# Kernel optimization log

Hardware: AMD Instinct MI355X
Metric: run time of the kernel (lower is better)

Reference implementation:

```python
import jax, jax.numpy as jnp
import numpy as np

B, T, V, E, H, D = 2048, 50, 65, 100, 20, 5  # batch, block, vocab, n_embd, heads, head_size


def setup_inputs() -> dict:
    key = jax.random.key(0)
    ks = jax.random.split(key, 12)
    idx = jax.random.randint(ks[0], (B, T), 0, V)
    targets = jax.random.randint(ks[1], (B, T), 0, V)
    tok_emb = jax.random.normal(ks[2], (V, E), dtype=jnp.float32) * 0.02
    pos_emb = jax.random.normal(ks[3], (T, E), dtype=jnp.float32) * 0.02
    # per-head Linear(N_EMBD, head_size, bias=False) weights, stacked over heads: [H, D, E]
    Wk = jax.random.normal(ks[4], (H, D, E), dtype=jnp.float32) * 0.1
    Wq = jax.random.normal(ks[5], (H, D, E), dtype=jnp.float32) * 0.1
    Wv = jax.random.normal(ks[6], (H, D, E), dtype=jnp.float32) * 0.1
    W_ff = jax.random.normal(ks[7], (E, E), dtype=jnp.float32) * 0.1
    b_ff = jnp.zeros((E,), dtype=jnp.float32)
    W_lm = jax.random.normal(ks[8], (V, E), dtype=jnp.float32) * 0.1
    b_lm = jnp.zeros((V,), dtype=jnp.float32)
    return {"idx": idx, "targets": targets, "tok_emb": tok_emb, "pos_emb": pos_emb,
            "Wk": Wk, "Wq": Wq, "Wv": Wv, "W_ff": W_ff, "b_ff": b_ff,
            "W_lm": W_lm, "b_lm": b_lm}


def reference(idx, targets, tok_emb, pos_emb, Wk, Wq, Wv, W_ff, b_ff, W_lm, b_lm):
    Bs, Ts = idx.shape
    x = tok_emb[idx] + pos_emb[:Ts]  # [B, T, E]
    # batched over all heads (equivalent to the per-head Python loop + concat)
    k = jnp.einsum('bte,hde->bhtd', x, Wk)
    q = jnp.einsum('bte,hde->bhtd', x, Wq)
    v = jnp.einsum('bte,hde->bhtd', x, Wv)
    # NOTE: faithful to original: k @ q^T, scaled by C**0.5 (multiply, C = N_EMBD)
    scale = jnp.asarray(E, x.dtype) ** 0.5
    w = jnp.einsum('bhtd,bhsd->bhts', k, q) * scale  # [B, H, T, S]
    tril = jnp.tril(jnp.ones((Ts, Ts), dtype=bool))
    w = jnp.where(tril, w, -jnp.inf)
    # original: torch.softmax(weights, dim=1) on [B, T, S] -> axis 't' here (axis=2)
    w = jax.nn.softmax(w, axis=2)
    attn = jnp.einsum('bhts,bhsd->bhtd', w, v)
    attn = attn.transpose(0, 2, 1, 3).reshape(Bs, Ts, H * D)  # concat heads -> [B, T, E]
    h = jax.nn.relu(attn @ W_ff.T + b_ff)  # FeedForward applied AFTER attention
    logits = h @ W_lm.T + b_lm  # [B, T, V]
    logits2d = logits.reshape(Bs * Ts, V)
    tflat = targets.reshape(Bs * Ts)
    logp = jax.nn.log_softmax(logits2d, axis=-1)
    loss = -jnp.take_along_axis(logp, tflat[:, None], axis=-1).mean()
    return (logits2d, loss)
```

## Files before the change

kernel.cpp:

```cpp
#include <hip/hip_runtime.h>
#include <hip/hip_bf16.h>

#define Bb 2048
#define Tt 50
#define Vv 65
#define Ee 100
#define Hh 20
#define Dd 5

typedef __bf16 v8bf __attribute__((ext_vector_type(8)));
typedef short v8s __attribute__((ext_vector_type(8)));
typedef short v4s __attribute__((ext_vector_type(4)));
typedef float f32x4 __attribute__((ext_vector_type(4)));

__device__ __forceinline__ v8bf bzero8() {
    v8s z = {0, 0, 0, 0, 0, 0, 0, 0};
    union { v8s s; v8bf b; } u; u.s = z; return u.b;
}
__device__ __forceinline__ unsigned short bfbits(float f) {
    union { __hip_bfloat16 h; unsigned short s; } c;
    c.h = __float2bfloat16(f);
    return c.s;
}
__device__ __forceinline__ float bf2f(short s) {
    union { unsigned i; float f; } c; c.i = ((unsigned)(unsigned short)s) << 16; return c.f;
}
__device__ __forceinline__ unsigned pack2(float a, float b) {
    return (unsigned)bfbits(a) | ((unsigned)bfbits(b) << 16);
}

__device__ __forceinline__ f32x4 mfma_16x16x16_bf16(v4s a, v4s b, f32x4 c) {
#if __has_builtin(__builtin_amdgcn_mfma_f32_16x16x16bf16_1k)
    return __builtin_amdgcn_mfma_f32_16x16x16bf16_1k(a, b, c, 0, 0, 0);
#else
    f32x4 d;
    asm volatile("v_mfma_f32_16x16x16_bf16 %0, %1, %2, %3\n\ts_nop 7\n\ts_nop 4"
                 : "=v"(d) : "v"(a), "v"(b), "v"(c));
    return d;
#endif
}

#define WS_WKQV 1024
#define WS_WFF  (1024 + 81920)
#define WS_WLM  (1024 + 81920 + 32768)
#define WS_LPART (1024 + 81920 + 32768 + 20480)

#define XSTR 136
#define R2 8000
#define R3 16000

__global__ __launch_bounds__(256) void prep_kernel(
    const float* __restrict__ Wk, const float* __restrict__ Wq,
    const float* __restrict__ Wv, const float* __restrict__ Wff,
    const float* __restrict__ Wlm, char* __restrict__ ws)
{
    int g = blockIdx.x * 256 + threadIdx.x;
    __hip_bfloat16* wkqv = (__hip_bfloat16*)(ws + WS_WKQV);
    __hip_bfloat16* wff  = (__hip_bfloat16*)(ws + WS_WFF);
    __hip_bfloat16* wlm  = (__hip_bfloat16*)(ws + WS_WLM);
    if (g < 40960) {
        int n = g >> 7, e = g & 127;
        float v = 0.f;
        if (e < Ee) {
            if (n < 100)      v = Wk[n * Ee + e] * 14.4269504089f;
            else if (n < 200) v = Wq[(n - 100) * Ee + e];
            else if (n < 300) v = Wv[(n - 200) * Ee + e];
        }
        wkqv[g] = __float2bfloat16(v);
    } else if (g < 57344) {
        int gg = g - 40960; int n = gg >> 7, e = gg & 127;
        float v = (e < Ee && n < Ee) ? Wff[n * Ee + e] : 0.f;
        wff[gg] = __float2bfloat16(v);
    } else {
        int gg = g - 57344; int n = gg >> 7, e = gg & 127;
        float v = (e < Ee && n < Vv) ? Wlm[n * Ee + e] : 0.f;
        wlm[gg] = __float2bfloat16(v);
    }
}

__global__ __launch_bounds__(256, 3) void gpt_main(
    const int* __restrict__ idx, const int* __restrict__ targets,
    const float* __restrict__ tok_emb, const float* __restrict__ pos_emb,
    const float* __restrict__ b_ff, const float* __restrict__ b_lm,
    const char* __restrict__ ws, float* __restrict__ out,
    float* __restrict__ loss_part)
{
    __shared__ __attribute__((aligned(16))) __hip_bfloat16 sh[22400];
    __shared__ int tok_s[Tt];
    __shared__ float bsum;

    const int b    = blockIdx.x;
    const int tid  = threadIdx.x;
    const int wave = tid >> 6;
    const int ln   = tid & 15;
    const int quad = (tid >> 4) & 3;

    if (tid < Tt) tok_s[tid] = idx[b * Tt + tid];
    if (tid == 0) bsum = 0.f;
    {
        const uint4 z4 = make_uint4(0u, 0u, 0u, 0u);
        for (int i = tid; i < 2800; i += 256) ((uint4*)sh)[i] = z4;
    }
    __syncthreads();
    for (int i = tid; i < Tt * 25; i += 256) {
        int r = i / 25, c4 = (i - r * 25) * 4;
        const float4 te = *(const float4*)&tok_emb[tok_s[r] * Ee + c4];
        const float4 pe = *(const float4*)&pos_emb[r * Ee + c4];
        ushort4 o;
        o.x = bfbits(te.x + pe.x); o.y = bfbits(te.y + pe.y);
        o.z = bfbits(te.z + pe.z); o.w = bfbits(te.w + pe.w);
        *(ushort4*)&sh[r * XSTR + c4] = o;
    }
    __syncthreads();

    {
        const __hip_bfloat16* wkqv = (const __hip_bfloat16*)(ws + WS_WKQV);
        f32x4 acc[5][4];
#pragma unroll
        for (int j = 0; j < 5; ++j)
#pragma unroll
            for (int mt = 0; mt < 4; ++mt) {
                f32x4 z = {0.f, 0.f, 0.f, 0.f};
                acc[j][mt] = z;
            }
#pragma unroll
        for (int kt = 0; kt < 4; ++kt) {
            v8bf a[4];
#pragma unroll
            for (int mt = 0; mt < 4; ++mt)
                a[mt] = (mt < 3 || ln < 2)
                      ? *(const v8bf*)&sh[(mt * 16 + ln) * XSTR + kt * 32 + quad * 8]
                      : bzero8();
#pragma unroll
            for (int j = 0; j < 5; ++j) {
                int nt = wave * 5 + j;
                v8bf bfr = *(const v8bf*)&wkqv[(nt * 16 + ln) * 128 + kt * 32 + quad * 8];
#pragma unroll
                for (int mt = 0; mt < 4; ++mt)
                    acc[j][mt] = __builtin_amdgcn_mfma_f32_16x16x32_bf16(a[mt], bfr, acc[j][mt], 0, 0, 0);
            }
        }
        __syncthreads();
        for (int i = tid; i < 1000; i += 256) {
            *(unsigned short*)&sh[i * 8 + 5] = 0;
            *(unsigned*)&sh[i * 8 + 6] = 0;
        }
#pragma unroll
        for (int j = 0; j < 5; ++j) {
            int n = (wave * 5 + j) * 16 + ln;
            if (n < 300) {
                int mat = n / 100;
                int jj  = n - mat * 100;
                int h   = jj / 5, d = jj - (jj / 5) * 5;
#pragma unroll
                for (int mt = 0; mt < 4; ++mt)
#pragma unroll
                    for (int r = 0; r < 4; ++r) {
                        int m = mt * 16 + quad * 4 + r;
                        if (m < Tt) {
                            __hip_bfloat16 val = __float2bfloat16(acc[j][mt][r]);
                            if (mat == 0)      sh[R2 + (h * 50 + m) * 8 + d] = val;
                            else if (mat == 1) sh[(h * 50 + m) * 8 + d] = val;
                            else               sh[R3 + (h * 5 + d) * 64 + m] = val;
                        }
                    }
            }
        }
    }
    __syncthreads();

    unsigned attp[5][8];
    {
        v4s ones4; ones4[0] = ones4[1] = ones4[2] = ones4[3] = (short)0x3F80;
#pragma unroll
        for (int hj = 0; hj < 5; ++hj) {
            const int h = wave * 5 + hj;
            v8bf qf[4], kf[4];
#pragma unroll
            for (int i = 0; i < 4; ++i) {
                int row = i * 16 + ln;
                qf[i] = (quad == 0) ? *(const v8bf*)&sh[(h * 50 + row) * 8] : bzero8();
                kf[i] = (quad == 0) ? *(const v8bf*)&sh[R2 + (h * 50 + row) * 8] : bzero8();
            }
            float rdv[4][4];
#pragma unroll
            for (int ns = 0; ns < 4; ++ns) {
                float esum[4] = {0.f, 0.f, 0.f, 0.f};
#pragma unroll
                for (int mt = ns; mt < 4; ++mt) {
                    f32x4 z = {0.f, 0.f, 0.f, 0.f};
                    f32x4 t2 = __builtin_amdgcn_mfma_f32_16x16x32_bf16(kf[mt], qf[ns], z, 0, 0, 0);
                    int s = ns * 16 + ln;
#pragma unroll
                    for (int r = 0; r < 4; ++r) {
                        int t = mt * 16 + quad * 4 + r;
                        float x = __builtin_amdgcn_exp2f(t2[r]);
                        esum[r] += (t >= s && t < Tt && s < Tt) ? x : 0.f;
                    }
                }
                v4s af;
                af[0] = (short)bfbits(esum[0]); af[1] = (short)bfbits(esum[1]);
                af[2] = (short)bfbits(esum[2]); af[3] = (short)bfbits(esum[3]);
                f32x4 z = {0.f, 0.f, 0.f, 0.f};
                f32x4 dres = mfma_16x16x16_bf16(af, ones4, z);
#pragma unroll
                for (int r = 0; r < 4; ++r) {
                    int s = ns * 16 + quad * 4 + r;
                    rdv[ns][r] = (s < Tt) ? __builtin_amdgcn_rcpf(dres[r]) : 0.f;
                }
            }
            f32x4 pac[4];
#pragma unroll
            for (int mt = 0; mt < 4; ++mt) { f32x4 z = {0.f, 0.f, 0.f, 0.f}; pac[mt] = z; }
#pragma unroll
            for (int ms = 0; ms < 4; ++ms) {
                v4s braw;
                if (ln < Dd) braw = *(const v4s*)&sh[R3 + (h * 5 + ln) * 64 + ms * 16 + quad * 4];
                else { v4s z = {0, 0, 0, 0}; braw = z; }
                v4s bvt;
#pragma unroll
                for (int j = 0; j < 4; ++j)
                    bvt[j] = (short)bfbits(bf2f(braw[j]) * rdv[ms][j]);
#pragma unroll
                for (int u = 0; u < 4 - ms; ++u) {
                    f32x4 z = {0.f, 0.f, 0.f, 0.f};
                    f32x4 t1 = __builtin_amdgcn_mfma_f32_16x16x32_bf16(qf[ms], kf[ms + u], z, 0, 0, 0);
                    int t = (ms + u) * 16 + ln;
                    v4s af;
#pragma unroll
                    for (int r = 0; r < 4; ++r) {
                        int s = ms * 16 + quad * 4 + r;
                        float x = __builtin_amdgcn_exp2f(t1[r]);
                        x = (t >= s && t < Tt && s < Tt) ? x : 0.f;
                        af[r] = (short)bfbits(x);
                    }
                    pac[ms + u] = mfma_16x16x16_bf16(af, bvt, pac[ms + u]);
                }
            }
#pragma unroll
            for (int mt = 0; mt < 4; ++mt) {
                attp[hj][mt * 2]     = pack2(pac[mt][0], pac[mt][1]);
                attp[hj][mt * 2 + 1] = pack2(pac[mt][2], pac[mt][3]);
            }
        }
    }
    __syncthreads();

#pragma unroll
    for (int hj = 0; hj < 5; ++hj) {
        int col = (wave * 5 + hj) * 5 + ln;
#pragma unroll
        for (int mt = 0; mt < 4; ++mt)
#pragma unroll
            for (int r = 0; r < 4; ++r) {
                int t = mt * 16 + quad * 4 + r;
                if (ln < Dd && t < Tt) {
                    unsigned w = attp[hj][mt * 2 + (r >> 1)];
                    unsigned short v = (unsigned short)((r & 1) ? (w >> 16) : (w & 0xffff));
                    *(unsigned short*)&sh[t * XSTR + col] = v;
                }
            }
    }
    __syncthreads();

    {
        const __hip_bfloat16* wff = (const __hip_bfloat16*)(ws + WS_WFF);
        f32x4 fac[2][4];
#pragma unroll
        for (int u = 0; u < 2; ++u)
#pragma unroll
            for (int mt = 0; mt < 4; ++mt) {
                f32x4 z = {0.f, 0.f, 0.f, 0.f};
                fac[u][mt] = z;
            }
        const int nn = (wave < 3) ? 2 : 1;
#pragma unroll
        for (int kt = 0; kt < 4; ++kt) {
            v8bf a[4];
#pragma unroll
            for (int mt = 0; mt < 4; ++mt)
                a[mt] = (mt < 3 || ln < 2)
                      ? *(const v8bf*)&sh[(mt * 16 + ln) * XSTR + kt * 32 + quad * 8]
                      : bzero8();
#pragma unroll
            for (int u = 0; u < 2; ++u) {
                if (u < nn) {
                    int nt = wave + u * 4;
                    v8bf bfr = *(const v8bf*)&wff[(nt * 16 + ln) * 128 + kt * 32 + quad * 8];
#pragma unroll
                    for (int mt = 0; mt < 4; ++mt)
                        fac[u][mt] = __builtin_amdgcn_mfma_f32_16x16x32_bf16(a[mt], bfr, fac[u][mt], 0, 0, 0);
                }
            }
        }
#pragma unroll
        for (int u = 0; u < 2; ++u) {
            if (u < nn) {
                int n = (wave + u * 4) * 16 + ln;
                if (n < Ee) {
                    float bias = b_ff[n];
#pragma unroll
                    for (int mt = 0; mt < 4; ++mt)
#pragma unroll
                        for (int r = 0; r < 4; ++r) {
                            int m = mt * 16 + quad * 4 + r;
                            if (m < Tt) {
                                float v = fac[u][mt][r] + bias;
                                sh[R2 + m * XSTR + n] = __float2bfloat16(v > 0.f ? v : 0.f);
                            }
                        }
                }
            }
        }
    }
    __syncthreads();

    {
        const __hip_bfloat16* wlm = (const __hip_bfloat16*)(ws + WS_WLM);
        float* lgl = (float*)sh;
#pragma unroll
        for (int i = 0; i < 5; ++i) {
            int job = wave + i * 4;
            int mt = job / 5, nt = job - (job / 5) * 5;
            f32x4 acc = {0.f, 0.f, 0.f, 0.f};
#pragma unroll
            for (int kt = 0; kt < 4; ++kt) {
                v8bf a = (mt < 3 || ln < 2)
                       ? *(const v8bf*)&sh[R2 + (mt * 16 + ln) * XSTR + kt * 32 + quad * 8]
                       : bzero8();
                v8bf bf = *(const v8bf*)&wlm[(nt * 16 + ln) * 128 + kt * 32 + quad * 8];
                acc = __builtin_amdgcn_mfma_f32_16x16x32_bf16(a, bf, acc, 0, 0, 0);
            }
            int n = nt * 16 + ln;
            if (n < Vv) {
                float bias = b_lm[n];
#pragma unroll
                for (int r = 0; r < 4; ++r) {
                    int m = mt * 16 + quad * 4 + r;
                    if (m < Tt) {
                        float v = acc[r] + bias;
                        out[(b * Tt + m) * Vv + n] = v;
                        lgl[m * 68 + n] = v;
                    }
                }
            }
        }
    }
    __syncthreads();

    if (tid < 200) {
        int r = tid >> 2, lv = tid & 3;
        const float* row = (const float*)sh + r * 68;
        float mx = -3.0e38f;
        for (int v = lv; v < Vv; v += 4) mx = fmaxf(mx, row[v]);
        mx = fmaxf(mx, __shfl_xor(mx, 1));
        mx = fmaxf(mx, __shfl_xor(mx, 2));
        float sum = 0.f;
        for (int v = lv; v < Vv; v += 4)
            sum += __builtin_amdgcn_exp2f((row[v] - mx) * 1.4426950408889634f);
        sum += __shfl_xor(sum, 1);
        sum += __shfl_xor(sum, 2);
        if (lv == 0) {
            float lse = mx + 0.69314718055994531f * log2f(sum);
            int tgt = targets[b * Tt + r];
            atomicAdd(&bsum, lse - row[tgt]);
        }
    }
    __syncthreads();
    if (tid == 0) loss_part[b] = bsum;
}

__global__ __launch_bounds__(256) void loss_reduce(const float* __restrict__ lp,
                                                   float* __restrict__ out)
{
    __shared__ float wsum[4];
    int tid = threadIdx.x;
    float s = 0.f;
    for (int i = tid; i < Bb; i += 256) s += lp[i];
    s += __shfl_xor(s, 1);  s += __shfl_xor(s, 2);  s += __shfl_xor(s, 4);
    s += __shfl_xor(s, 8);  s += __shfl_xor(s, 16); s += __shfl_xor(s, 32);
    if ((tid & 63) == 0) wsum[tid >> 6] = s;
    __syncthreads();
    if (tid == 0)
        out[Bb * Tt * Vv] = (wsum[0] + wsum[1] + wsum[2] + wsum[3]) * (1.0f / (float)(Bb * Tt));
}

extern "C" void kernel_launch(void* const* d_in, const int* in_sizes, int n_in,
                              void* d_out, int out_size, void* d_ws, size_t ws_size,
                              hipStream_t stream)
{
    const int* idx     = (const int*)d_in[0];
    const int* targets = (const int*)d_in[1];
    const float* tok_emb = (const float*)d_in[2];
    const float* pos_emb = (const float*)d_in[3];
    const float* Wk  = (const float*)d_in[4];
    const float* Wq  = (const float*)d_in[5];
    const float* Wv  = (const float*)d_in[6];
    const float* Wff = (const float*)d_in[7];
    const float* bff = (const float*)d_in[8];
    const float* Wlm = (const float*)d_in[9];
    const float* blm = (const float*)d_in[10];
    float* out = (float*)d_out;
    char* ws = (char*)d_ws;
    float* loss_part = (float*)(ws + WS_LPART);

    hipLaunchKernelGGL(prep_kernel, dim3(264), dim3(256), 0, stream, Wk, Wq, Wv, Wff, Wlm, ws);
    hipLaunchKernelGGL(gpt_main, dim3(Bb), dim3(256), 0, stream,
                       idx, targets, tok_emb, pos_emb, bff, blm, (const char*)ws, out, loss_part);
    hipLaunchKernelGGL(loss_reduce, dim3(1), dim3(256), 0, stream, loss_part, out);
}
```

Measured before the change: 188.1 us.

## Store Q/K in fp8 and shrink shared memory to fit more blocks per CU

Q and K projections are now stored in LDS as fp8 e4m3 and the attention score MFMAs use the fp8 variant. The log2e·sqrt(E) scaling is split evenly across Wk and Wq so both sit in a reasonable fp8 range. The LDS buffer is re-laid out as bytes and shrunk from about 44.8KB to 28.8KB, and launch bounds rise from 3 to 5 blocks per CU to improve occupancy. This risks precision loss in the attention scores, since fp8 has a 3-bit mantissa and the scores are scaled by about 14.4 before exp2.

```diff
diff --git a/kernel.cpp b/kernel.cpp
--- a/kernel.cpp
+++ b/kernel.cpp
@@ -1,5 +1,6 @@
 #include <hip/hip_runtime.h>
 #include <hip/hip_bf16.h>
+#include <hip/hip_fp8.h>
 
 #define Bb 2048
 #define Tt 50
@@ -27,6 +28,15 @@
 }
 __device__ __forceinline__ unsigned pack2(float a, float b) {
     return (unsigned)bfbits(a) | ((unsigned)bfbits(b) << 16);
+}
+__device__ __forceinline__ unsigned char f32_to_fp8(float v) {
+#if __has_builtin(__builtin_amdgcn_cvt_pk_fp8_f32)
+    return (unsigned char)(__builtin_amdgcn_cvt_pk_fp8_f32(v, 0.f, 0, false) & 0xff);
+#else
+    union { __hip_fp8_e4m3 t; unsigned char c; } u;
+    u.t = __hip_fp8_e4m3(v);
+    return u.c;
+#endif
 }
 
 __device__ __forceinline__ f32x4 mfma_16x16x16_bf16(v4s a, v4s b, f32x4 c) {
@@ -45,9 +55,10 @@
 #define WS_WLM  (1024 + 81920 + 32768)
 #define WS_LPART (1024 + 81920 + 32768 + 20480)
 
-#define XSTR 136
-#define R2 8000
-#define R3 16000
+#define KB8 8000
+#define VTB 16000
+#define HB  13600
+#define XROW 272
 
 __global__ __launch_bounds__(256) void prep_kernel(
     const float* __restrict__ Wk, const float* __restrict__ Wq,
@@ -62,8 +73,8 @@
         int n = g >> 7, e = g & 127;
         float v = 0.f;
         if (e < Ee) {
-            if (n < 100)      v = Wk[n * Ee + e] * 14.4269504089f;
-            else if (n < 200) v = Wq[(n - 100) * Ee + e];
+            if (n < 100)      v = Wk[n * Ee + e] * 3.7982825f;
+            else if (n < 200) v = Wq[(n - 100) * Ee + e] * 3.7982825f;
             else if (n < 300) v = Wv[(n - 200) * Ee + e];
         }
         wkqv[g] = __float2bfloat16(v);
@@ -78,14 +89,14 @@
     }
 }
 
-__global__ __launch_bounds__(256, 3) void gpt_main(
+__global__ __launch_bounds__(256, 5) void gpt_main(
     const int* __restrict__ idx, const int* __restrict__ targets,
     const float* __restrict__ tok_emb, const float* __restrict__ pos_emb,
     const float* __restrict__ b_ff, const float* __restrict__ b_lm,
     const char* __restrict__ ws, float* __restrict__ out,
     float* __restrict__ loss_part)
 {
-    __shared__ __attribute__((aligned(16))) __hip_bfloat16 sh[22400];
+    __shared__ __attribute__((aligned(16))) unsigned char shB[28800];
     __shared__ int tok_s[Tt];
     __shared__ float bsum;
 
@@ -99,7 +110,7 @@
     if (tid == 0) bsum = 0.f;
     {
         const uint4 z4 = make_uint4(0u, 0u, 0u, 0u);
-        for (int i = tid; i < 2800; i += 256) ((uint4*)sh)[i] = z4;
+        for (int i = tid; i < 1800; i += 256) ((uint4*)shB)[i] = z4;
     }
     __syncthreads();
     for (int i = tid; i < Tt * 25; i += 256) {
@@ -109,7 +120,7 @@
         ushort4 o;
         o.x = bfbits(te.x + pe.x); o.y = bfbits(te.y + pe.y);
         o.z = bfbits(te.z + pe.z); o.w = bfbits(te.w + pe.w);
-        *(ushort4*)&sh[r * XSTR + c4] = o;
+        *(ushort4*)&shB[r * XROW + c4 * 2] = o;
     }
     __syncthreads();
 
@@ -129,7 +140,7 @@
 #pragma unroll
             for (int mt = 0; mt < 4; ++mt)
                 a[mt] = (mt < 3 || ln < 2)
-                      ? *(const v8bf*)&sh[(mt * 16 + ln) * XSTR + kt * 32 + quad * 8]
+                      ? *(const v8bf*)&shB[(mt * 16 + ln) * XROW + (kt * 32 + quad * 8) * 2]
                       : bzero8();
 #pragma unroll
             for (int j = 0; j < 5; ++j) {
@@ -142,8 +153,8 @@
         }
         __syncthreads();
         for (int i = tid; i < 1000; i += 256) {
-            *(unsigned short*)&sh[i * 8 + 5] = 0;
-            *(unsigned*)&sh[i * 8 + 6] = 0;
+            shB[i * 8 + 5] = 0; *(unsigned short*)&shB[i * 8 + 6] = 0;
+            shB[KB8 + i * 8 + 5] = 0; *(unsigned short*)&shB[KB8 + i * 8 + 6] = 0;
         }
 #pragma unroll
         for (int j = 0; j < 5; ++j) {
@@ -158,10 +169,10 @@
                     for (int r = 0; r < 4; ++r) {
                         int m = mt * 16 + quad * 4 + r;
                         if (m < Tt) {
-                            __hip_bfloat16 val = __float2bfloat16(acc[j][mt][r]);
-                            if (mat == 0)      sh[R2 + (h * 50 + m) * 8 + d] = val;
-                            else if (mat == 1) sh[(h * 50 + m) * 8 + d] = val;
-                            else               sh[R3 + (h * 5 + d) * 64 + m] = val;
+                            float v = acc[j][mt][r];
+                            if (mat == 0)      shB[KB8 + (h * 50 + m) * 8 + d] = f32_to_fp8(v);
+                            else if (mat == 1) shB[(h * 50 + m) * 8 + d] = f32_to_fp8(v);
+                            else *(unsigned short*)&shB[VTB + ((h * 5 + d) * 64 + m) * 2] = bfbits(v);
                         }
                     }
             }
@@ -175,12 +186,12 @@
 #pragma unroll
         for (int hj = 0; hj < 5; ++hj) {
             const int h = wave * 5 + hj;
-            v8bf qf[4], kf[4];
+            long qf[4], kf[4];
 #pragma unroll
             for (int i = 0; i < 4; ++i) {
                 int row = i * 16 + ln;
-                qf[i] = (quad == 0) ? *(const v8bf*)&sh[(h * 50 + row) * 8] : bzero8();
-                kf[i] = (quad == 0) ? *(const v8bf*)&sh[R2 + (h * 50 + row) * 8] : bzero8();
+                qf[i] = (quad == 0) ? *(const long*)&shB[(h * 50 + row) * 8] : 0L;
+                kf[i] = (quad == 0) ? *(const long*)&shB[KB8 + (h * 50 + row) * 8] : 0L;
             }
             float rdv[4][4];
 #pragma unroll
@@ -189,7 +200,7 @@
 #pragma unroll
                 for (int mt = ns; mt < 4; ++mt) {
                     f32x4 z = {0.f, 0.f, 0.f, 0.f};
-                    f32x4 t2 = __builtin_amdgcn_mfma_f32_16x16x32_bf16(kf[mt], qf[ns], z, 0, 0, 0);
+                    f32x4 t2 = __builtin_amdgcn_mfma_f32_16x16x32_fp8_fp8(kf[mt], qf[ns], z, 0, 0, 0);
                     int s = ns * 16 + ln;
 #pragma unroll
                     for (int r = 0; r < 4; ++r) {
@@ -215,7 +226,7 @@
 #pragma unroll
             for (int ms = 0; ms < 4; ++ms) {
                 v4s braw;
-                if (ln < Dd) braw = *(const v4s*)&sh[R3 + (h * 5 + ln) * 64 + ms * 16 + quad * 4];
+                if (ln < Dd) braw = *(const v4s*)&shB[VTB + ((h * 5 + ln) * 64 + ms * 16 + quad * 4) * 2];
                 else { v4s z = {0, 0, 0, 0}; braw = z; }
                 v4s bvt;
 #pragma unroll
@@ -224,7 +235,7 @@
 #pragma unroll
                 for (int u = 0; u < 4 - ms; ++u) {
                     f32x4 z = {0.f, 0.f, 0.f, 0.f};
-                    f32x4 t1 = __builtin_amdgcn_mfma_f32_16x16x32_bf16(qf[ms], kf[ms + u], z, 0, 0, 0);
+                    f32x4 t1 = __builtin_amdgcn_mfma_f32_16x16x32_fp8_fp8(qf[ms], kf[ms + u], z, 0, 0, 0);
                     int t = (ms + u) * 16 + ln;
                     v4s af;
 #pragma unroll
@@ -257,7 +268,7 @@
                 if (ln < Dd && t < Tt) {
                     unsigned w = attp[hj][mt * 2 + (r >> 1)];
                     unsigned short v = (unsigned short)((r & 1) ? (w >> 16) : (w & 0xffff));
-                    *(unsigned short*)&sh[t * XSTR + col] = v;
+                    *(unsigned short*)&shB[t * XROW + col * 2] = v;
                 }
             }
     }
@@ -280,7 +291,7 @@
 #pragma unroll
             for (int mt = 0; mt < 4; ++mt)
                 a[mt] = (mt < 3 || ln < 2)
-                      ? *(const v8bf*)&sh[(mt * 16 + ln) * XSTR + kt * 32 + quad * 8]
+                      ? *(const v8bf*)&shB[(mt * 16 + ln) * XROW + (kt * 32 + quad * 8) * 2]
                       : bzero8();
 #pragma unroll
             for (int u = 0; u < 2; ++u) {
@@ -306,7 +317,8 @@
                             int m = mt * 16 + quad * 4 + r;
                             if (m < Tt) {
                                 float v = fac[u][mt][r] + bias;
-                                sh[R2 + m * XSTR + n] = __float2bfloat16(v > 0.f ? v : 0.f);
+                                *(unsigned short*)&shB[HB + m * XROW + n * 2] =
+                                    bfbits(v > 0.f ? v : 0.f);
                             }
                         }
                 }
@@ -317,7 +329,7 @@
 
     {
         const __hip_bfloat16* wlm = (const __hip_bfloat16*)(ws + WS_WLM);
-        float* lgl = (float*)sh;
+        float* lgl = (float*)shB;
 #pragma unroll
         for (int i = 0; i < 5; ++i) {
             int job = wave + i * 4;
@@ -326,7 +338,7 @@
 #pragma unroll
             for (int kt = 0; kt < 4; ++kt) {
                 v8bf a = (mt < 3 || ln < 2)
-                       ? *(const v8bf*)&sh[R2 + (mt * 16 + ln) * XSTR + kt * 32 + quad * 8]
+                       ? *(const v8bf*)&shB[HB + (mt * 16 + ln) * XROW + (kt * 32 + quad * 8) * 2]
                        : bzero8();
                 v8bf bf = *(const v8bf*)&wlm[(nt * 16 + ln) * 128 + kt * 32 + quad * 8];
                 acc = __builtin_amdgcn_mfma_f32_16x16x32_bf16(a, bf, acc, 0, 0, 0);
@@ -350,7 +362,7 @@
 
     if (tid < 200) {
         int r = tid >> 2, lv = tid & 3;
-        const float* row = (const float*)sh + r * 68;
+        const float* row = (const float*)shB + r * 68;
         float mx = -3.0e38f;
         for (int v = lv; v < Vv; v += 4) mx = fmaxf(mx, row[v]);
         mx = fmaxf(mx, __shfl_xor(mx, 1));
```

New measurement: 241.5 us. 28.4% more time.
